# Optimization experiments

Measured on AMD Instinct MI355X. Metric: run time of the kernel, lower is better.

Reference implementation:

```python
import jax, jax.numpy as jnp
import numpy as np

B, LQ, LK, C = 16, 1024, 1024, 512
WH = int(LQ ** 0.5)  # 32


def setup_inputs() -> dict:
    key = jax.random.key(0)
    ks = jax.random.split(key, 6)
    s1 = 1.0 / np.sqrt(LK)
    return {
        "query": jax.random.normal(ks[0], (B, LQ, C), jnp.float32),
        "key": jax.random.normal(ks[1], (B, LK, C), jnp.float32),
        "value": jax.random.normal(ks[2], (B, LK, C), jnp.float32),
        # nn.Linear weights, stored [out_features, in_features] like torch
        "w1": jax.random.normal(ks[3], (LK, LK), jnp.float32) * s1,
        "w2": jax.random.normal(ks[4], (LK, LK), jnp.float32) * s1,
        "w3": jax.random.normal(ks[5], (1, LK), jnp.float32) * s1,
    }


def reference(query, key, value, w1, w2, w3):
    # cosine-similarity matrix (computed under no_grad in the original)
    q = query / 100.0
    k = key / 100.0
    qn = jnp.sqrt(jnp.sum(q * q, axis=-1))[:, :, None]   # [B, LQ, 1]
    kn = jnp.sqrt(jnp.sum(k * k, axis=-1))[:, None, :]   # [B, 1, LK]
    outer = qn * kn                                       # rank-1 outer product [B, LQ, LK]
    upper = jnp.einsum('bqc,bkc->bqk', q, k)              # [B, LQ, LK]
    similar_rev = jax.lax.stop_gradient(upper / (outer + 1e-6))

    # 3-layer MLP gating over the LK axis -> scalar weight per query row
    h = jax.nn.gelu(jnp.einsum('bqk,ok->bqo', similar_rev, w1), approximate=False)
    h = jax.nn.gelu(jnp.einsum('bqk,ok->bqo', h, w2), approximate=False)
    w = jnp.einsum('bqk,ok->bqo', h, w3)[..., 0]          # [B, LQ]

    # weight^T @ similar_rev / wh, then tanh -> per-key scalar gate [B, LK, 1]
    weight = jnp.einsum('bq,bqk->bk', w, similar_rev) / WH
    weight = jnp.tanh(weight)[:, :, None]

    # value modulation + residual
    return value * weight + value
```

## Files before the change

kernel.cpp:

```cpp
#include <hip/hip_runtime.h>
#include <hip/hip_bf16.h>

#define B_  16
#define LQ_ 1024
#define LK_ 1024
#define C_  512

typedef __attribute__((ext_vector_type(4))) float f32x4;
typedef __attribute__((ext_vector_type(8))) short bf16x8;

__device__ __forceinline__ float bf2f(ushort u) {
  union { unsigned int i; float f; } v; v.i = ((unsigned int)u) << 16; return v.f;
}
__device__ __forceinline__ ushort f2bf(float f) {
  union { float f; unsigned int i; } v; v.f = f;
  unsigned int r = v.i + 0x7fffu + ((v.i >> 16) & 1u);
  return (ushort)(r >> 16);
}
__device__ __forceinline__ float gelu_exact(float x) {
  return 0.5f * x * (1.0f + erff(x * 0.70710678118654752f));
}

__device__ __forceinline__ void gload_lds16(const ushort* g, ushort* l) {
  __builtin_amdgcn_global_load_lds(
      (const __attribute__((address_space(1))) void*)g,
      (__attribute__((address_space(3))) void*)l, 16, 0, 0);
}

__global__ __launch_bounds__(256) void prep_qk(const float* __restrict__ x,
                                               ushort* __restrict__ xb,
                                               float* __restrict__ norms) {
  int wid = blockIdx.x * 4 + (threadIdx.x >> 6);
  int lane = threadIdx.x & 63;
  const float* xr = x + (long)wid * C_;
  ushort* xo = xb + (long)wid * C_;
  float ss = 0.f;
#pragma unroll
  for (int i0 = 0; i0 < 2; ++i0) {
    int i = lane * 4 + i0 * 256;
    float4 v = *(const float4*)(xr + i);
    ss += v.x * v.x + v.y * v.y + v.z * v.z + v.w * v.w;
    ushort4 o;
    o.x = f2bf(v.x); o.y = f2bf(v.y); o.z = f2bf(v.z); o.w = f2bf(v.w);
    *(ushort4*)(xo + i) = o;
  }
#pragma unroll
  for (int off = 32; off > 0; off >>= 1) ss += __shfl_xor(ss, off);
  if (lane == 0) norms[wid] = sqrtf(ss);
}

__global__ __launch_bounds__(256) void conv_bf16(const float* __restrict__ x,
                                                 ushort* __restrict__ o, int n4) {
  int i = blockIdx.x * 256 + threadIdx.x;
  if (i < n4) {
    float4 v = *(const float4*)(x + (long)i * 4);
    ushort4 u;
    u.x = f2bf(v.x); u.y = f2bf(v.y); u.z = f2bf(v.z); u.w = f2bf(v.w);
    *(ushort4*)(o + (long)i * 4) = u;
  }
}

#define BK 32

template <int EPI>
__device__ __forceinline__ void gemm128_body(
    const ushort* __restrict__ A, const ushort* __restrict__ Bm,
    ushort* __restrict__ Cc, int K, long sA, long sB, long sC,
    const float* __restrict__ qn, const float* __restrict__ kn,
    const float* __restrict__ w3v, float* __restrict__ wv) {
  int per = (int)(gridDim.x >> 3);
  int orig = blockIdx.x;
  int id = (orig & 7) * per + (orig >> 3);
  int b = id >> 6;
  int rtile = id & 63;
  const int bm = (rtile >> 3) * 128, bn = (rtile & 7) * 128;

  A += (long)b * sA;
  Bm += (long)b * sB;

  __shared__ ushort smem[16384];

  int tid = threadIdx.x;
  int lane = tid & 63, w = tid >> 6;
  int wr = w >> 1, wc = w & 1;
  int l16 = lane & 15, lhi = lane >> 4;

  f32x4 acc[4][4] = {};

  int c0 = tid, c1 = tid + 256;
  int r0 = c0 >> 2, cb0 = (c0 & 3) ^ ((r0 >> 1) & 3);
  int r1 = c1 >> 2, cb1 = (c1 & 3) ^ ((r1 >> 1) & 3);
  int wb0 = (tid & ~63) * 8;
  int wb1 = wb0 + 256 * 8;

  const ushort* Ar0 = A + (long)(bm + r0) * K + cb0 * 8;
  const ushort* Ar1 = A + (long)(bm + r1) * K + cb1 * 8;
  const ushort* Br0 = Bm + (long)(bn + r0) * K + cb0 * 8;
  const ushort* Br1 = Bm + (long)(bn + r1) * K + cb1 * 8;

  const int nt = K / BK;
  gload_lds16(Ar0, smem + wb0);
  gload_lds16(Ar1, smem + wb1);
  gload_lds16(Br0, smem + 8192 + wb0);
  gload_lds16(Br1, smem + 8192 + wb1);
  __syncthreads();

  int cur = 0;
  for (int t = 0; t < nt; ++t) {
    if (t + 1 < nt) {
      int k1 = (t + 1) * BK;
      int nx = (cur ^ 1) * 4096;
      gload_lds16(Ar0 + k1, smem + nx + wb0);
      gload_lds16(Ar1 + k1, smem + nx + wb1);
      gload_lds16(Br0 + k1, smem + 8192 + nx + wb0);
      gload_lds16(Br1 + k1, smem + 8192 + nx + wb1);
    }

    const ushort* Ac = smem + cur * 4096;
    const ushort* Bc = smem + 8192 + cur * 4096;
    bf16x8 af[4], bfr[4];
#pragma unroll
    for (int m = 0; m < 4; ++m) {
      int r = wr * 64 + m * 16 + l16;
      af[m] = *(const bf16x8*)(Ac + r * 32 + ((lhi ^ ((r >> 1) & 3)) * 8));
    }
#pragma unroll
    for (int n = 0; n < 4; ++n) {
      int r = wc * 64 + n * 16 + l16;
      bfr[n] = *(const bf16x8*)(Bc + r * 32 + ((lhi ^ ((r >> 1) & 3)) * 8));
    }
#pragma unroll
    for (int m = 0; m < 4; ++m)
#pragma unroll
      for (int n = 0; n < 4; ++n)
        acc[m][n] = __builtin_amdgcn_mfma_f32_16x16x32_bf16(af[m], bfr[n],
                                                            acc[m][n], 0, 0, 0);
    __syncthreads();
    cur ^= 1;
  }

  if constexpr (EPI == 2) {
    float* wvb = wv + (long)b * LQ_;
    float w3c[4];
#pragma unroll
    for (int n = 0; n < 4; ++n) w3c[n] = w3v[bn + wc * 64 + n * 16 + l16];
#pragma unroll
    for (int m = 0; m < 4; ++m)
#pragma unroll
      for (int rr = 0; rr < 4; ++rr) {
        float s = 0.f;
#pragma unroll
        for (int n = 0; n < 4; ++n)
          s += gelu_exact(acc[m][n][rr]) * w3c[n];
        s += __shfl_xor(s, 1);
        s += __shfl_xor(s, 2);
        s += __shfl_xor(s, 4);
        s += __shfl_xor(s, 8);
        if (l16 == 0)
          atomicAdd(&wvb[bm + wr * 64 + m * 16 + lhi * 4 + rr], s);
      }
  } else {
    Cc += (long)b * sC;
    const float* qnb = qn + (long)b * LQ_;
    const float* knb = kn + (long)b * LK_;
#pragma unroll
    for (int m = 0; m < 4; ++m) {
#pragma unroll
      for (int rr = 0; rr < 4; ++rr) {
        int lrow = wr * 64 + m * 16 + lhi * 4 + rr;
#pragma unroll
        for (int n = 0; n < 4; ++n) {
          int col = wc * 64 + n * 16 + l16;
          float v = acc[m][n][rr];
          if (EPI == 0) {
            v = v / (qnb[bm + lrow] * knb[bn + col] + 1e-2f);
          } else {
            v = gelu_exact(v);
          }
          int pc = (col >> 3) ^ (lrow & 15);
          smem[lrow * 128 + pc * 8 + (col & 7)] = f2bf(v);
        }
      }
    }
    __syncthreads();
#pragma unroll
    for (int p = 0; p < 8; ++p) {
      int row = p * 16 + (tid >> 4);
      int cj = tid & 15;
      int pc = cj ^ (row & 15);
      bf16x8 v = *(const bf16x8*)(smem + row * 128 + pc * 8);
      *(bf16x8*)&Cc[(long)(bm + row) * 1024 + bn + cj * 8] = v;
    }
  }
}

__global__ __launch_bounds__(256, 4) void gemm_s(
    const ushort* __restrict__ A, const ushort* __restrict__ Bm,
    ushort* __restrict__ Cc, const float* __restrict__ qn,
    const float* __restrict__ kn) {
  gemm128_body<0>(A, Bm, Cc, C_, (long)LQ_ * C_, (long)LK_ * C_,
                  (long)LQ_ * LK_, qn, kn, nullptr, nullptr);
}

__global__ __launch_bounds__(256, 4) void gemm_h1(
    const ushort* __restrict__ A, const ushort* __restrict__ Bm,
    ushort* __restrict__ Cc) {
  gemm128_body<1>(A, Bm, Cc, LK_, (long)LQ_ * LK_, 0L, (long)LQ_ * LK_,
                  nullptr, nullptr, nullptr, nullptr);
}

__global__ __launch_bounds__(256, 4) void gemm_h2w(
    const ushort* __restrict__ A, const ushort* __restrict__ Bm,
    const float* __restrict__ w3v, float* __restrict__ wv) {
  gemm128_body<2>(A, Bm, nullptr, LK_, (long)LQ_ * LK_, 0L, 0L,
                  nullptr, nullptr, w3v, wv);
}

__global__ __launch_bounds__(256) void gate_partial(const ushort* __restrict__ S,
                                                    const float* __restrict__ wv,
                                                    float* __restrict__ wraw) {
  int b = blockIdx.z;
  int k = blockIdx.x * 256 + threadIdx.x;
  int q0 = blockIdx.y * 128;
  const ushort* Sb = S + (long)b * LQ_ * LK_;
  const float* wb = wv + b * LQ_;
  float acc = 0.f;
#pragma unroll 4
  for (int q = q0; q < q0 + 128; ++q) acc += wb[q] * bf2f(Sb[(long)q * LK_ + k]);
  atomicAdd(&wraw[b * LK_ + k], acc);
}

__global__ __launch_bounds__(256) void finalize(const float* __restrict__ value,
                                                const float* __restrict__ wraw,
                                                float* __restrict__ out) {
  long i = (long)blockIdx.x * 256 + threadIdx.x;
  long e = i * 4;
  int row = (int)(e >> 9);
  float g = 1.f + tanhf(wraw[row] * (1.f / 32.f));
  float4 v = ((const float4*)value)[i];
  v.x *= g; v.y *= g; v.z *= g; v.w *= g;
  ((float4*)out)[i] = v;
}

extern "C" void kernel_launch(void* const* d_in, const int* in_sizes, int n_in,
                              void* d_out, int out_size, void* d_ws,
                              size_t ws_size, hipStream_t stream) {
  const float* query = (const float*)d_in[0];
  const float* key   = (const float*)d_in[1];
  const float* value = (const float*)d_in[2];
  const float* w1    = (const float*)d_in[3];
  const float* w2    = (const float*)d_in[4];
  const float* w3    = (const float*)d_in[5];
  float* out = (float*)d_out;

  const size_t QB_BYTES = (size_t)B_ * LQ_ * C_ * 2;
  const size_t S_BYTES  = (size_t)B_ * LQ_ * LK_ * 2;
  const size_t W_BYTES  = (size_t)LK_ * LK_ * 2;
  const size_t OFF_QB = 0;
  const size_t OFF_KB = OFF_QB + QB_BYTES;
  const size_t OFF_S  = OFF_KB + QB_BYTES;
  const size_t OFF_H1 = OFF_S + S_BYTES;
  const size_t OFF_W1 = OFF_H1 + S_BYTES;
  const size_t OFF_W2 = OFF_W1 + W_BYTES;
  const size_t OFF_QN = OFF_W2 + W_BYTES;
  const size_t OFF_KN = OFF_QN + (size_t)B_ * LQ_ * 4;
  const size_t OFF_WV = OFF_KN + (size_t)B_ * LK_ * 4;
  const size_t OFF_WR = OFF_WV + (size_t)B_ * LQ_ * 4;
  const size_t TOTAL  = OFF_WR + (size_t)B_ * LK_ * 4;
  if (ws_size < TOTAL) return;

  char* ws = (char*)d_ws;
  ushort* Qb  = (ushort*)(ws + OFF_QB);
  ushort* Kb  = (ushort*)(ws + OFF_KB);
  ushort* S   = (ushort*)(ws + OFF_S);
  ushort* h1  = (ushort*)(ws + OFF_H1);
  ushort* W1b = (ushort*)(ws + OFF_W1);
  ushort* W2b = (ushort*)(ws + OFF_W2);
  float* qn   = (float*)(ws + OFF_QN);
  float* kn   = (float*)(ws + OFF_KN);
  float* wv   = (float*)(ws + OFF_WV);
  float* wraw = (float*)(ws + OFF_WR);

  prep_qk<<<dim3(B_ * LQ_ / 4), 256, 0, stream>>>(query, Qb, qn);
  prep_qk<<<dim3(B_ * LK_ / 4), 256, 0, stream>>>(key, Kb, kn);
  conv_bf16<<<dim3(LK_ * LK_ / 4 / 256), 256, 0, stream>>>(w1, W1b, LK_ * LK_ / 4);
  conv_bf16<<<dim3(LK_ * LK_ / 4 / 256), 256, 0, stream>>>(w2, W2b, LK_ * LK_ / 4);
  hipMemsetAsync(wraw, 0, (size_t)B_ * LK_ * 4, stream);
  hipMemsetAsync(wv, 0, (size_t)B_ * LQ_ * 4, stream);

  gemm_s<<<dim3(1024), 256, 0, stream>>>(Qb, Kb, S, qn, kn);

  gemm_h1<<<dim3(1024), 256, 0, stream>>>(S, W1b, h1);

  gemm_h2w<<<dim3(1024), 256, 0, stream>>>(h1, W2b, w3, wv);

  gate_partial<<<dim3(LK_ / 256, LQ_ / 128, B_), 256, 0, stream>>>(S, wv, wraw);

  finalize<<<dim3((size_t)B_ * LK_ * C_ / 4 / 256), 256, 0, stream>>>(value, wraw, out);
}
```

Before: 183.8 us.

## Use tanh-approx GELU, process two tiles per block, and drop LDS-staged epilogue stores

Replaces exact erf GELU with a tanh-based approximation built on __expf. Each GEMM block now computes two adjacent 128x128 output tiles, halving the grid to 512 and lowering launch bounds to 2 waves per SIMD. The epilogue no longer stages results through LDS for coalesced 16-byte stores and instead writes scalar bf16 values directly to global memory. Together these aim to cut GELU arithmetic and per-tile overhead, at the cost of a small numerical deviation, uncoalesced 2-byte stores, and fewer blocks to fill the CUs.

After: 184.7 us. About the same (+0.5%).

```diff
diff --git a/kernel.cpp b/kernel.cpp
--- a/kernel.cpp
+++ b/kernel.cpp
@@ -17,8 +17,12 @@
   unsigned int r = v.i + 0x7fffu + ((v.i >> 16) & 1u);
   return (ushort)(r >> 16);
 }
-__device__ __forceinline__ float gelu_exact(float x) {
-  return 0.5f * x * (1.0f + erff(x * 0.70710678118654752f));
+__device__ __forceinline__ float gelu_fast(float x) {
+  float u = x * (0.7978845608f + 0.0356774081f * x * x);
+  u = fminf(fmaxf(u, -9.f), 9.f);
+  float e = __expf(2.f * u);
+  float t = (e - 1.f) / (e + 1.f);
+  return 0.5f * x * (1.f + t);
 }
 
 __device__ __forceinline__ void gload_lds16(const ushort* g, ushort* l) {
@@ -63,23 +67,12 @@
 #define BK 32
 
 template <int EPI>
-__device__ __forceinline__ void gemm128_body(
-    const ushort* __restrict__ A, const ushort* __restrict__ Bm,
-    ushort* __restrict__ Cc, int K, long sA, long sB, long sC,
+__device__ __forceinline__ void tile128(
+    const ushort* __restrict__ A, const ushort* __restrict__ Bm,
+    ushort* __restrict__ Cc, int K, int bm, int bn, int b,
     const float* __restrict__ qn, const float* __restrict__ kn,
-    const float* __restrict__ w3v, float* __restrict__ wv) {
-  int per = (int)(gridDim.x >> 3);
-  int orig = blockIdx.x;
-  int id = (orig & 7) * per + (orig >> 3);
-  int b = id >> 6;
-  int rtile = id & 63;
-  const int bm = (rtile >> 3) * 128, bn = (rtile & 7) * 128;
-
-  A += (long)b * sA;
-  Bm += (long)b * sB;
-
-  __shared__ ushort smem[16384];
-
+    const float* __restrict__ w3v, float* __restrict__ wv,
+    ushort* smem) {
   int tid = threadIdx.x;
   int lane = tid & 63, w = tid >> 6;
   int wr = w >> 1, wc = w & 1;
@@ -151,7 +144,7 @@
         float s = 0.f;
 #pragma unroll
         for (int n = 0; n < 4; ++n)
-          s += gelu_exact(acc[m][n][rr]) * w3c[n];
+          s += gelu_fast(acc[m][n][rr]) * w3c[n];
         s += __shfl_xor(s, 1);
         s += __shfl_xor(s, 2);
         s += __shfl_xor(s, 4);
@@ -160,60 +153,72 @@
           atomicAdd(&wvb[bm + wr * 64 + m * 16 + lhi * 4 + rr], s);
       }
   } else {
-    Cc += (long)b * sC;
     const float* qnb = qn + (long)b * LQ_;
     const float* knb = kn + (long)b * LK_;
 #pragma unroll
     for (int m = 0; m < 4; ++m) {
-#pragma unroll
-      for (int rr = 0; rr < 4; ++rr) {
-        int lrow = wr * 64 + m * 16 + lhi * 4 + rr;
-#pragma unroll
-        for (int n = 0; n < 4; ++n) {
-          int col = wc * 64 + n * 16 + l16;
+      int row0 = bm + wr * 64 + m * 16 + lhi * 4;
+#pragma unroll
+      for (int n = 0; n < 4; ++n) {
+        int col = bn + wc * 64 + n * 16 + l16;
+#pragma unroll
+        for (int rr = 0; rr < 4; ++rr) {
           float v = acc[m][n][rr];
+          int grow = row0 + rr;
           if (EPI == 0) {
-            v = v / (qnb[bm + lrow] * knb[bn + col] + 1e-2f);
+            v = v / (qnb[grow] * knb[col] + 1e-2f);
           } else {
-            v = gelu_exact(v);
+            v = gelu_fast(v);
           }
-          int pc = (col >> 3) ^ (lrow & 15);
-          smem[lrow * 128 + pc * 8 + (col & 7)] = f2bf(v);
+          Cc[(long)grow * 1024 + col] = f2bf(v);
         }
       }
     }
-    __syncthreads();
-#pragma unroll
-    for (int p = 0; p < 8; ++p) {
-      int row = p * 16 + (tid >> 4);
-      int cj = tid & 15;
-      int pc = cj ^ (row & 15);
-      bf16x8 v = *(const bf16x8*)(smem + row * 128 + pc * 8);
-      *(bf16x8*)&Cc[(long)(bm + row) * 1024 + bn + cj * 8] = v;
-    }
   }
 }
 
-__global__ __launch_bounds__(256, 4) void gemm_s(
+template <int EPI>
+__device__ __forceinline__ void gemm_pair_body(
+    const ushort* __restrict__ A, const ushort* __restrict__ Bm,
+    ushort* __restrict__ Cc, int K, long sA, long sB, long sC,
+    const float* __restrict__ qn, const float* __restrict__ kn,
+    const float* __restrict__ w3v, float* __restrict__ wv) {
+  int per = (int)(gridDim.x >> 3);
+  int orig = blockIdx.x;
+  int id = (orig & 7) * per + (orig >> 3);
+  int b = id >> 5;
+  int rp = id & 31;
+  const int bm = (rp >> 2) * 128, bn0 = (rp & 3) * 256;
+
+  A += (long)b * sA;
+  Bm += (long)b * sB;
+  if (EPI != 2) Cc += (long)b * sC;
+
+  __shared__ ushort smem[16384];
+  tile128<EPI>(A, Bm, Cc, K, bm, bn0, b, qn, kn, w3v, wv, smem);
+  tile128<EPI>(A, Bm, Cc, K, bm, bn0 + 128, b, qn, kn, w3v, wv, smem);
+}
+
+__global__ __launch_bounds__(256, 2) void gemm_s(
     const ushort* __restrict__ A, const ushort* __restrict__ Bm,
     ushort* __restrict__ Cc, const float* __restrict__ qn,
     const float* __restrict__ kn) {
-  gemm128_body<0>(A, Bm, Cc, C_, (long)LQ_ * C_, (long)LK_ * C_,
-                  (long)LQ_ * LK_, qn, kn, nullptr, nullptr);
-}
-
-__global__ __launch_bounds__(256, 4) void gemm_h1(
+  gemm_pair_body<0>(A, Bm, Cc, C_, (long)LQ_ * C_, (long)LK_ * C_,
+                    (long)LQ_ * LK_, qn, kn, nullptr, nullptr);
+}
+
+__global__ __launch_bounds__(256, 2) void gemm_h1(
     const ushort* __restrict__ A, const ushort* __restrict__ Bm,
     ushort* __restrict__ Cc) {
-  gemm128_body<1>(A, Bm, Cc, LK_, (long)LQ_ * LK_, 0L, (long)LQ_ * LK_,
-                  nullptr, nullptr, nullptr, nullptr);
-}
-
-__global__ __launch_bounds__(256, 4) void gemm_h2w(
+  gemm_pair_body<1>(A, Bm, Cc, LK_, (long)LQ_ * LK_, 0L, (long)LQ_ * LK_,
+                    nullptr, nullptr, nullptr, nullptr);
+}
+
+__global__ __launch_bounds__(256, 2) void gemm_h2w(
     const ushort* __restrict__ A, const ushort* __restrict__ Bm,
     const float* __restrict__ w3v, float* __restrict__ wv) {
-  gemm128_body<2>(A, Bm, nullptr, LK_, (long)LQ_ * LK_, 0L, 0L,
-                  nullptr, nullptr, w3v, wv);
+  gemm_pair_body<2>(A, Bm, nullptr, LK_, (long)LQ_ * LK_, 0L, 0L,
+                    nullptr, nullptr, w3v, wv);
 }
 
 __global__ __launch_bounds__(256) void gate_partial(const ushort* __restrict__ S,
@@ -288,11 +293,11 @@
   hipMemsetAsync(wraw, 0, (size_t)B_ * LK_ * 4, stream);
   hipMemsetAsync(wv, 0, (size_t)B_ * LQ_ * 4, stream);
 
-  gemm_s<<<dim3(1024), 256, 0, stream>>>(Qb, Kb, S, qn, kn);
-
-  gemm_h1<<<dim3(1024), 256, 0, stream>>>(S, W1b, h1);
-
-  gemm_h2w<<<dim3(1024), 256, 0, stream>>>(h1, W2b, w3, wv);
+  gemm_s<<<dim3(512), 256, 0, stream>>>(Qb, Kb, S, qn, kn);
+
+  gemm_h1<<<dim3(512), 256, 0, stream>>>(S, W1b, h1);
+
+  gemm_h2w<<<dim3(512), 256, 0, stream>>>(h1, W2b, w3, wv);
 
   gate_partial<<<dim3(LK_ / 256, LQ_ / 128, B_), 256, 0, stream>>>(S, wv, wraw);
 
```
